# Optimization experiments

Hardware: AMD Instinct MI355X
Metric: run time of the kernel (lower is better)

## Reference

```python
import jax, jax.numpy as jnp
import numpy as np

INV_SQRT2 = 0.7071067811865476  # Haar/db1 filter coefficient
LEVEL = 3


def _split(x, axis):
    """One Haar analysis step along `axis` (even length assumed)."""
    ax = axis % x.ndim
    sl0 = [slice(None)] * x.ndim; sl0[ax] = slice(0, None, 2)
    sl1 = [slice(None)] * x.ndim; sl1[ax] = slice(1, None, 2)
    x0, x1 = x[tuple(sl0)], x[tuple(sl1)]
    return (x0 + x1) * INV_SQRT2, (x0 - x1) * INV_SQRT2


def _merge(lo, hi, axis):
    """One Haar synthesis step along `axis` (interleave even/odd)."""
    ax = axis % lo.ndim
    e = (lo + hi) * INV_SQRT2
    o = (lo - hi) * INV_SQRT2
    s = jnp.stack([e, o], axis=ax + 1)
    shape = list(lo.shape)
    shape[ax] *= 2
    return s.reshape(shape)


def _dwt2(x):
    lo, hi = _split(x, -1)
    a, h = _split(lo, -2)
    v, d = _split(hi, -2)
    return a, h, v, d


def _idwt2(a, h, v, d):
    lo = _merge(a, h, -2)
    hi = _merge(v, d, -2)
    return _merge(lo, hi, -1)


def setup_inputs() -> dict:
    key = jax.random.key(0)
    ks = jax.random.split(key, 8)
    B, H, W = 16, 1024, 1024
    x = jax.random.normal(ks[0], (B, H, W, 1), dtype=jnp.float32)
    na = (H // 8) * (W // 8)   # approx size at level 3
    n2 = (H // 4) * (W // 4)
    n1 = (H // 2) * (W // 2)
    scale = 0.02
    Wa = jax.random.normal(ks[1], (na, 1), dtype=jnp.float32) * scale
    ba = jnp.zeros((1,), jnp.float32)
    Wd1 = jax.random.normal(ks[2], (3 * na, 3), dtype=jnp.float32) * scale  # coarsest details
    bd1 = jnp.zeros((3,), jnp.float32)
    Wd2 = jax.random.normal(ks[3], (3 * n2, 3), dtype=jnp.float32) * scale
    bd2 = jnp.zeros((3,), jnp.float32)
    Wd3 = jax.random.normal(ks[4], (3 * n1, 3), dtype=jnp.float32) * scale  # finest details
    bd3 = jnp.zeros((3,), jnp.float32)
    return {"x": x, "Wa": Wa, "ba": ba, "Wd1": Wd1, "bd1": bd1,
            "Wd2": Wd2, "bd2": bd2, "Wd3": Wd3, "bd3": bd3}


def reference(x, Wa, ba, Wd1, bd1, Wd2, bd2, Wd3, bd3):
    img = x[..., 0]                      # [B, H, W]
    B = img.shape[0]
    details = []                         # finest -> coarsest
    cur = img
    for _ in range(LEVEL):
        cur, h, v, d = _dwt2(cur)
        details.append((h, v, d))
    # approximation attention: sigmoid(Dense(1)) scalar gate per sample
    aw = jax.nn.sigmoid(cur.reshape(B, -1) @ Wa + ba)   # [B, 1]
    rec = cur * aw[:, :, None]                           # [B, H/8, W/8]
    # detail attention per level (coarsest first, matching pywt coeff order)
    det_params = [(Wd1, bd1), (Wd2, bd2), (Wd3, bd3)]
    for (h, v, d), (Wd, bd) in zip(reversed(details), det_params):
        flat = jnp.stack([h, v, d], axis=1).reshape(B, -1)      # [B, 3*hl*wl]
        w = jax.nn.softmax(flat @ Wd + bd, axis=-1)             # [B, 3]
        rec = _idwt2(rec,
                     h * w[:, 0, None, None],
                     v * w[:, 1, None, None],
                     d * w[:, 2, None, None])
    return rec                                                   # [B, H, W]
```

## Files before the change

kernel.cpp:

```cpp
#include <hip/hip_runtime.h>
#include <math.h>

#define HH 1024
#define WW 1024
#define N1 262144
#define N2 65536
#define N3 16384
#define NCHUNK 4
#define ROWS_PER_IMG 512

#define C_INV_SQRT2 0.70710678118654752440f

static __device__ __forceinline__ void haar_fwd(float P, float Q, float R, float S,
                                                float& a, float& h, float& v, float& d) {
    const float C = C_INV_SQRT2;
    float lo0 = (P + Q) * C, lo1 = (R + S) * C;
    float hi0 = (P - Q) * C, hi1 = (R - S) * C;
    a = (lo0 + lo1) * C; h = (lo0 - lo1) * C;
    v = (hi0 + hi1) * C; d = (hi0 - hi1) * C;
}

static __device__ __forceinline__ void haar_inv(float a, float h, float v, float d,
                                                float& P, float& Q, float& R, float& S) {
    const float C = C_INV_SQRT2;
    float elo = (a + h) * C, olo = (a - h) * C;
    float ehi = (v + d) * C, ohi = (v - d) * C;
    P = (elo + ehi) * C; Q = (elo - ehi) * C;
    R = (olo + ohi) * C; S = (olo - ohi) * C;
}

__global__ __launch_bounds__(256) void wa_fwd_dots(
    const float* __restrict__ x,
    const float* __restrict__ Wa,
    const float* __restrict__ Wd1,
    const float* __restrict__ Wd2,
    const float* __restrict__ Wd3,
    float* __restrict__ partial,
    int ipc)
{
    const int strip = blockIdx.x;
    const int chunk = blockIdx.y;
    const int t = threadIdx.x;
    const int lane = t & 63, wave = t >> 6;

    float w1[3][4][6];
    #pragma unroll
    for (int qr = 0; qr < 4; ++qr) {
        const size_t jj = (size_t)(strip * 4 + qr) * 512 + 2 * t;
        #pragma unroll
        for (int s = 0; s < 3; ++s) {
            const float2* src = (const float2*)(Wd3 + (jj + (size_t)s * N1) * 3);
            float2 f0 = src[0], f1 = src[1], f2 = src[2];
            w1[s][qr][0] = f0.x; w1[s][qr][1] = f0.y; w1[s][qr][2] = f1.x;
            w1[s][qr][3] = f1.y; w1[s][qr][4] = f2.x; w1[s][qr][5] = f2.y;
        }
    }
    float w2[3][2][3];
    #pragma unroll
    for (int QR = 0; QR < 2; ++QR) {
        const size_t jj = (size_t)(strip * 2 + QR) * 256 + t;
        #pragma unroll
        for (int s = 0; s < 3; ++s) {
            const float* src = Wd2 + (jj + (size_t)s * N2) * 3;
            w2[s][QR][0] = src[0]; w2[s][QR][1] = src[1]; w2[s][QR][2] = src[2];
        }
    }
    float w3[3][3] = {};
    float wa = 0.f;
    if (!(t & 1)) {
        const size_t jj = (size_t)strip * 128 + (t >> 1);
        wa = Wa[jj];
        #pragma unroll
        for (int s = 0; s < 3; ++s) {
            const float* src = Wd1 + (jj + (size_t)s * N3) * 3;
            w3[s][0] = src[0]; w3[s][1] = src[1]; w3[s][2] = src[2];
        }
    }

    #pragma unroll 2
    for (int bi = 0; bi < ipc; ++bi) {
        const int b = chunk * ipc + bi;
        const float* xr = x + (size_t)b * HH * WW + (size_t)strip * 8 * WW + 4 * t;

        float acc[10];
        #pragma unroll
        for (int c = 0; c < 10; ++c) acc[c] = 0.f;

        float a1[4][2];
        #pragma unroll
        for (int qr = 0; qr < 4; ++qr) {
            float4 u0 = *(const float4*)(xr + (size_t)(2 * qr)     * WW);
            float4 u1 = *(const float4*)(xr + (size_t)(2 * qr + 1) * WW);
            float h_[2], v_[2], d_[2];
            haar_fwd(u0.x, u0.y, u1.x, u1.y, a1[qr][0], h_[0], v_[0], d_[0]);
            haar_fwd(u0.z, u0.w, u1.z, u1.w, a1[qr][1], h_[1], v_[1], d_[1]);
            #pragma unroll
            for (int qc = 0; qc < 2; ++qc)
                #pragma unroll
                for (int c = 0; c < 3; ++c)
                    acc[7 + c] += h_[qc] * w1[0][qr][qc * 3 + c]
                                + v_[qc] * w1[1][qr][qc * 3 + c]
                                + d_[qc] * w1[2][qr][qc * 3 + c];
        }

        float a2[2];
        #pragma unroll
        for (int QR = 0; QR < 2; ++QR) {
            float h2, v2, d2;
            haar_fwd(a1[2 * QR][0], a1[2 * QR][1], a1[2 * QR + 1][0], a1[2 * QR + 1][1],
                     a2[QR], h2, v2, d2);
            #pragma unroll
            for (int c = 0; c < 3; ++c)
                acc[4 + c] += h2 * w2[0][QR][c] + v2 * w2[1][QR][c] + d2 * w2[2][QR][c];
        }

        {
            float oa0 = __shfl_xor(a2[0], 1);
            float oa1 = __shfl_xor(a2[1], 1);
            if (!(t & 1)) {
                float a3, h3, v3, d3;
                haar_fwd(a2[0], oa0, a2[1], oa1, a3, h3, v3, d3);
                acc[0] += a3 * wa;
                #pragma unroll
                for (int c = 0; c < 3; ++c)
                    acc[1 + c] += h3 * w3[0][c] + v3 * w3[1][c] + d3 * w3[2][c];
            }
        }

        #pragma unroll
        for (int c = 0; c < 10; ++c) {
            float s = acc[c];
            #pragma unroll
            for (int off = 1; off < 64; off <<= 1) s += __shfl_xor(s, off);
            acc[c] = s;
        }
        if (lane == 0) {
            float* row = partial + ((size_t)b * ROWS_PER_IMG + (size_t)strip * 4 + wave) * 10;
            #pragma unroll
            for (int c = 0; c < 10; ++c) row[c] = acc[c];
        }
    }
}

__global__ __launch_bounds__(64) void wa_gates(
    const float* __restrict__ partial,
    const float* __restrict__ ba,
    const float* __restrict__ bd1,
    const float* __restrict__ bd2,
    const float* __restrict__ bd3,
    float* __restrict__ gates)
{
    const int b = blockIdx.x;
    const int l = threadIdx.x;
    float v[10];
    #pragma unroll
    for (int c = 0; c < 10; ++c) v[c] = 0.f;
    for (int r = l; r < ROWS_PER_IMG; r += 64) {
        const float* row = partial + ((size_t)b * ROWS_PER_IMG + r) * 10;
        #pragma unroll
        for (int c = 0; c < 10; ++c) v[c] += row[c];
    }
    #pragma unroll
    for (int c = 0; c < 10; ++c) {
        #pragma unroll
        for (int off = 1; off < 64; off <<= 1) v[c] += __shfl_xor(v[c], off);
    }
    if (l == 0) {
        float* G = gates + b * 10;
        G[0] = 1.f / (1.f + expf(-(v[0] + ba[0])));
        const float* bds[3] = { bd1, bd2, bd3 };
        #pragma unroll
        for (int lv = 0; lv < 3; ++lv) {
            float l0 = v[1 + 3 * lv + 0] + bds[lv][0];
            float l1 = v[1 + 3 * lv + 1] + bds[lv][1];
            float l2 = v[1 + 3 * lv + 2] + bds[lv][2];
            float m = fmaxf(l0, fmaxf(l1, l2));
            float e0 = expf(l0 - m), e1 = expf(l1 - m), e2 = expf(l2 - m);
            float inv = 1.f / (e0 + e1 + e2);
            G[1 + 3 * lv + 0] = e0 * inv;
            G[1 + 3 * lv + 1] = e1 * inv;
            G[1 + 3 * lv + 2] = e2 * inv;
        }
    }
}

__global__ __launch_bounds__(256) void wa_recon(
    const float* __restrict__ x,
    const float* __restrict__ gates,
    float* __restrict__ out)
{
    const int strip = blockIdx.x;
    const int b = blockIdx.y;
    const int t = threadIdx.x;

    __shared__ float g[10];
    if (t < 10) g[t] = gates[b * 10 + t];
    __syncthreads();

    const float* xr = x + (size_t)b * HH * WW + (size_t)strip * 8 * WW + 4 * t;

    float a1[4][2], h1[4][2], v1[4][2], d1[4][2];
    #pragma unroll
    for (int qr = 0; qr < 4; ++qr) {
        float4 u0 = *(const float4*)(xr + (size_t)(2 * qr)     * WW);
        float4 u1 = *(const float4*)(xr + (size_t)(2 * qr + 1) * WW);
        haar_fwd(u0.x, u0.y, u1.x, u1.y, a1[qr][0], h1[qr][0], v1[qr][0], d1[qr][0]);
        haar_fwd(u0.z, u0.w, u1.z, u1.w, a1[qr][1], h1[qr][1], v1[qr][1], d1[qr][1]);
    }
    float a2[2], h2[2], v2[2], d2[2];
    #pragma unroll
    for (int QR = 0; QR < 2; ++QR)
        haar_fwd(a1[2 * QR][0], a1[2 * QR][1], a1[2 * QR + 1][0], a1[2 * QR + 1][1],
                 a2[QR], h2[QR], v2[QR], d2[QR]);

    float oa0 = __shfl_xor(a2[0], 1);
    float oa1 = __shfl_xor(a2[1], 1);
    const bool rightside = t & 1;
    float a3, h3, v3, d3;
    if (!rightside) haar_fwd(a2[0], oa0, a2[1], oa1, a3, h3, v3, d3);
    else            haar_fwd(oa0, a2[0], oa1, a2[1], a3, h3, v3, d3);

    a3 *= g[0];
    float P, Q, R, S;
    haar_inv(a3, h3 * g[1], v3 * g[2], d3 * g[3], P, Q, R, S);
    float r2[2];
    r2[0] = rightside ? Q : P;
    r2[1] = rightside ? S : R;

    float ra1[4][2];
    #pragma unroll
    for (int QR = 0; QR < 2; ++QR) {
        haar_inv(r2[QR], h2[QR] * g[4], v2[QR] * g[5], d2[QR] * g[6], P, Q, R, S);
        ra1[2 * QR][0] = P; ra1[2 * QR][1] = Q;
        ra1[2 * QR + 1][0] = R; ra1[2 * QR + 1][1] = S;
    }

    float* orow = out + (size_t)b * HH * WW + (size_t)strip * 8 * WW + 4 * t;
    #pragma unroll
    for (int qr = 0; qr < 4; ++qr) {
        float4 o0, o1;
        haar_inv(ra1[qr][0], h1[qr][0] * g[7], v1[qr][0] * g[8], d1[qr][0] * g[9],
                 o0.x, o0.y, o1.x, o1.y);
        haar_inv(ra1[qr][1], h1[qr][1] * g[7], v1[qr][1] * g[8], d1[qr][1] * g[9],
                 o0.z, o0.w, o1.z, o1.w);
        *(float4*)(orow + (size_t)(2 * qr)     * WW) = o0;
        *(float4*)(orow + (size_t)(2 * qr + 1) * WW) = o1;
    }
}

extern "C" void kernel_launch(void* const* d_in, const int* in_sizes, int n_in,
                              void* d_out, int out_size, void* d_ws, size_t ws_size,
                              hipStream_t stream) {
    const float* x   = (const float*)d_in[0];
    const float* Wa  = (const float*)d_in[1];
    const float* ba  = (const float*)d_in[2];
    const float* Wd1 = (const float*)d_in[3];
    const float* bd1 = (const float*)d_in[4];
    const float* Wd2 = (const float*)d_in[5];
    const float* bd2 = (const float*)d_in[6];
    const float* Wd3 = (const float*)d_in[7];
    const float* bd3 = (const float*)d_in[8];
    float* out = (float*)d_out;

    const int B = in_sizes[0] / (HH * WW);

    float* partial = (float*)d_ws;
    float* gates   = partial + (size_t)B * ROWS_PER_IMG * 10;

    int nchunk = NCHUNK, ipc = B / NCHUNK;
    if (B % NCHUNK) { nchunk = B; ipc = 1; }

    dim3 fgrid(128, nchunk);
    wa_fwd_dots<<<fgrid, 256, 0, stream>>>(x, Wa, Wd1, Wd2, Wd3, partial, ipc);
    wa_gates<<<B, 64, 0, stream>>>(partial, ba, bd1, bd2, bd3, gates);
    dim3 rgrid(128, B);
    wa_recon<<<rgrid, 256, 0, stream>>>(x, gates, out);
}
```

Measured before the change: 155.2 us.

## Fuse forward dots, gate computation and reconstruction into one cooperative kernel

Replaces the three-kernel sequence (forward dot products, gate softmax, reconstruction) with a single cooperative kernel that uses a grid-wide sync between the reduction phase and the reconstruction phase. Weights stay in registers, each block computes the gates for its own images redundantly after the sync, and then reconstructs directly. This removes two kernel launches and the separate gate kernel, at the cost of a grid barrier and a 512-block cooperative launch that must be fully co-resident. The old three-kernel path remains as a fallback if the cooperative launch fails.

```diff
diff --git a/kernel.cpp b/kernel.cpp
--- a/kernel.cpp
+++ b/kernel.cpp
@@ -1,4 +1,5 @@
 #include <hip/hip_runtime.h>
+#include <hip/hip_cooperative_groups.h>
 #include <math.h>
 
 #define HH 1024
@@ -8,8 +9,11 @@
 #define N3 16384
 #define NCHUNK 4
 #define ROWS_PER_IMG 512
+#define MAX_IPC 8
 
 #define C_INV_SQRT2 0.70710678118654752440f
+
+namespace cg = cooperative_groups;
 
 static __device__ __forceinline__ void haar_fwd(float P, float Q, float R, float S,
                                                 float& a, float& h, float& v, float& d) {
@@ -27,6 +31,232 @@
     float ehi = (v + d) * C, ohi = (v - d) * C;
     P = (elo + ehi) * C; Q = (elo - ehi) * C;
     R = (olo + ohi) * C; S = (olo - ohi) * C;
+}
+
+__global__ __launch_bounds__(256, 2) void wa_fused(
+    const float* __restrict__ x,
+    const float* __restrict__ Wa,
+    const float* __restrict__ ba,
+    const float* __restrict__ Wd1,
+    const float* __restrict__ bd1,
+    const float* __restrict__ Wd2,
+    const float* __restrict__ bd2,
+    const float* __restrict__ Wd3,
+    const float* __restrict__ bd3,
+    float* __restrict__ partial,
+    float* __restrict__ out,
+    int ipc)
+{
+    const int strip = blockIdx.x;
+    const int chunk = blockIdx.y;
+    const int t = threadIdx.x;
+    const int lane = t & 63, wave = t >> 6;
+
+    __shared__ float smP[MAX_IPC][16][10];
+    __shared__ float smG[2][10];
+    __shared__ float gl[10];
+
+    float w1[3][4][6];
+    #pragma unroll
+    for (int qr = 0; qr < 4; ++qr) {
+        const size_t jj = (size_t)(strip * 4 + qr) * 512 + 2 * t;
+        #pragma unroll
+        for (int s = 0; s < 3; ++s) {
+            const float2* src = (const float2*)(Wd3 + (jj + (size_t)s * N1) * 3);
+            float2 f0 = src[0], f1 = src[1], f2 = src[2];
+            w1[s][qr][0] = f0.x; w1[s][qr][1] = f0.y; w1[s][qr][2] = f1.x;
+            w1[s][qr][3] = f1.y; w1[s][qr][4] = f2.x; w1[s][qr][5] = f2.y;
+        }
+    }
+    float w2[3][2][3];
+    #pragma unroll
+    for (int QR = 0; QR < 2; ++QR) {
+        const size_t jj = (size_t)(strip * 2 + QR) * 256 + t;
+        #pragma unroll
+        for (int s = 0; s < 3; ++s) {
+            const float* src = Wd2 + (jj + (size_t)s * N2) * 3;
+            w2[s][QR][0] = src[0]; w2[s][QR][1] = src[1]; w2[s][QR][2] = src[2];
+        }
+    }
+    float w3[3][3] = {};
+    float wa = 0.f;
+    if (!(t & 1)) {
+        const size_t jj = (size_t)strip * 128 + (t >> 1);
+        wa = Wa[jj];
+        #pragma unroll
+        for (int s = 0; s < 3; ++s) {
+            const float* src = Wd1 + (jj + (size_t)s * N3) * 3;
+            w3[s][0] = src[0]; w3[s][1] = src[1]; w3[s][2] = src[2];
+        }
+    }
+
+    #pragma unroll 2
+    for (int bi = 0; bi < ipc; ++bi) {
+        const int b = chunk * ipc + bi;
+        const float* xr = x + (size_t)b * HH * WW + (size_t)strip * 8 * WW + 4 * t;
+
+        float acc[10];
+        #pragma unroll
+        for (int c = 0; c < 10; ++c) acc[c] = 0.f;
+
+        float a1[4][2];
+        #pragma unroll
+        for (int qr = 0; qr < 4; ++qr) {
+            float4 u0 = *(const float4*)(xr + (size_t)(2 * qr)     * WW);
+            float4 u1 = *(const float4*)(xr + (size_t)(2 * qr + 1) * WW);
+            float h_[2], v_[2], d_[2];
+            haar_fwd(u0.x, u0.y, u1.x, u1.y, a1[qr][0], h_[0], v_[0], d_[0]);
+            haar_fwd(u0.z, u0.w, u1.z, u1.w, a1[qr][1], h_[1], v_[1], d_[1]);
+            #pragma unroll
+            for (int qc = 0; qc < 2; ++qc)
+                #pragma unroll
+                for (int c = 0; c < 3; ++c)
+                    acc[7 + c] += h_[qc] * w1[0][qr][qc * 3 + c]
+                                + v_[qc] * w1[1][qr][qc * 3 + c]
+                                + d_[qc] * w1[2][qr][qc * 3 + c];
+        }
+
+        float a2[2];
+        #pragma unroll
+        for (int QR = 0; QR < 2; ++QR) {
+            float h2, v2, d2;
+            haar_fwd(a1[2 * QR][0], a1[2 * QR][1], a1[2 * QR + 1][0], a1[2 * QR + 1][1],
+                     a2[QR], h2, v2, d2);
+            #pragma unroll
+            for (int c = 0; c < 3; ++c)
+                acc[4 + c] += h2 * w2[0][QR][c] + v2 * w2[1][QR][c] + d2 * w2[2][QR][c];
+        }
+
+        {
+            float oa0 = __shfl_xor(a2[0], 1);
+            float oa1 = __shfl_xor(a2[1], 1);
+            if (!(t & 1)) {
+                float a3, h3, v3, d3;
+                haar_fwd(a2[0], oa0, a2[1], oa1, a3, h3, v3, d3);
+                acc[0] += a3 * wa;
+                #pragma unroll
+                for (int c = 0; c < 3; ++c)
+                    acc[1 + c] += h3 * w3[0][c] + v3 * w3[1][c] + d3 * w3[2][c];
+            }
+        }
+
+        #pragma unroll
+        for (int c = 0; c < 10; ++c) {
+            float s = acc[c];
+            s += __shfl_xor(s, 1);
+            s += __shfl_xor(s, 2);
+            s += __shfl_xor(s, 4);
+            s += __shfl_xor(s, 8);
+            acc[c] = s;
+        }
+        const int sel = lane & 15;
+        float vsel = acc[0];
+        #pragma unroll
+        for (int c = 1; c < 10; ++c) vsel = (sel == c) ? acc[c] : vsel;
+        if (sel < 10) smP[bi][(wave << 2) | (lane >> 4)][sel] = vsel;
+    }
+    __syncthreads();
+    if (t < ipc * 10) {
+        const int bi = t / 10, c = t - bi * 10;
+        float s = 0.f;
+        #pragma unroll
+        for (int j = 0; j < 16; ++j) s += smP[bi][j][c];
+        partial[((size_t)(chunk * ipc + bi) * 128 + strip) * 10 + c] = s;
+    }
+
+    __threadfence();
+    cg::this_grid().sync();
+
+    for (int bi = 0; bi < ipc; ++bi) {
+        const int b = chunk * ipc + bi;
+
+        if (t < 128) {
+            const float* row = partial + ((size_t)b * 128 + t) * 10;
+            float v[10];
+            #pragma unroll
+            for (int c = 0; c < 10; ++c) v[c] = row[c];
+            #pragma unroll
+            for (int c = 0; c < 10; ++c) {
+                #pragma unroll
+                for (int off = 1; off < 64; off <<= 1) v[c] += __shfl_xor(v[c], off);
+            }
+            if (lane == 0) {
+                #pragma unroll
+                for (int c = 0; c < 10; ++c) smG[wave][c] = v[c];
+            }
+        }
+        __syncthreads();
+        if (t == 0) {
+            const float* bds[3] = { bd1, bd2, bd3 };
+            float s0 = smG[0][0] + smG[1][0];
+            gl[0] = 1.f / (1.f + expf(-(s0 + ba[0])));
+            #pragma unroll
+            for (int lv = 0; lv < 3; ++lv) {
+                float l0 = smG[0][1 + 3 * lv + 0] + smG[1][1 + 3 * lv + 0] + bds[lv][0];
+                float l1 = smG[0][1 + 3 * lv + 1] + smG[1][1 + 3 * lv + 1] + bds[lv][1];
+                float l2 = smG[0][1 + 3 * lv + 2] + smG[1][1 + 3 * lv + 2] + bds[lv][2];
+                float m = fmaxf(l0, fmaxf(l1, l2));
+                float e0 = expf(l0 - m), e1 = expf(l1 - m), e2 = expf(l2 - m);
+                float inv = 1.f / (e0 + e1 + e2);
+                gl[1 + 3 * lv + 0] = e0 * inv;
+                gl[1 + 3 * lv + 1] = e1 * inv;
+                gl[1 + 3 * lv + 2] = e2 * inv;
+            }
+        }
+        __syncthreads();
+        float gv[10];
+        #pragma unroll
+        for (int c = 0; c < 10; ++c) gv[c] = gl[c];
+
+        const float* xr = x + (size_t)b * HH * WW + (size_t)strip * 8 * WW + 4 * t;
+        float a1r[4][2], h1[4][2], v1[4][2], d1[4][2];
+        #pragma unroll
+        for (int qr = 0; qr < 4; ++qr) {
+            float4 u0 = *(const float4*)(xr + (size_t)(2 * qr)     * WW);
+            float4 u1 = *(const float4*)(xr + (size_t)(2 * qr + 1) * WW);
+            haar_fwd(u0.x, u0.y, u1.x, u1.y, a1r[qr][0], h1[qr][0], v1[qr][0], d1[qr][0]);
+            haar_fwd(u0.z, u0.w, u1.z, u1.w, a1r[qr][1], h1[qr][1], v1[qr][1], d1[qr][1]);
+        }
+        float a2r[2], h2[2], v2[2], d2[2];
+        #pragma unroll
+        for (int QR = 0; QR < 2; ++QR)
+            haar_fwd(a1r[2 * QR][0], a1r[2 * QR][1], a1r[2 * QR + 1][0], a1r[2 * QR + 1][1],
+                     a2r[QR], h2[QR], v2[QR], d2[QR]);
+
+        float oa0 = __shfl_xor(a2r[0], 1);
+        float oa1 = __shfl_xor(a2r[1], 1);
+        const bool rightside = t & 1;
+        float a3, h3, v3, d3;
+        if (!rightside) haar_fwd(a2r[0], oa0, a2r[1], oa1, a3, h3, v3, d3);
+        else            haar_fwd(oa0, a2r[0], oa1, a2r[1], a3, h3, v3, d3);
+
+        a3 *= gv[0];
+        float P, Q, R, S;
+        haar_inv(a3, h3 * gv[1], v3 * gv[2], d3 * gv[3], P, Q, R, S);
+        float r2[2];
+        r2[0] = rightside ? Q : P;
+        r2[1] = rightside ? S : R;
+
+        float ra1[4][2];
+        #pragma unroll
+        for (int QR = 0; QR < 2; ++QR) {
+            haar_inv(r2[QR], h2[QR] * gv[4], v2[QR] * gv[5], d2[QR] * gv[6], P, Q, R, S);
+            ra1[2 * QR][0] = P; ra1[2 * QR][1] = Q;
+            ra1[2 * QR + 1][0] = R; ra1[2 * QR + 1][1] = S;
+        }
+
+        float* orow = out + (size_t)b * HH * WW + (size_t)strip * 8 * WW + 4 * t;
+        #pragma unroll
+        for (int qr = 0; qr < 4; ++qr) {
+            float4 o0, o1;
+            haar_inv(ra1[qr][0], h1[qr][0] * gv[7], v1[qr][0] * gv[8], d1[qr][0] * gv[9],
+                     o0.x, o0.y, o1.x, o1.y);
+            haar_inv(ra1[qr][1], h1[qr][1] * gv[7], v1[qr][1] * gv[8], d1[qr][1] * gv[9],
+                     o0.z, o0.w, o1.z, o1.w);
+            *(float4*)(orow + (size_t)(2 * qr)     * WW) = o0;
+            *(float4*)(orow + (size_t)(2 * qr + 1) * WW) = o1;
+        }
+    }
 }
 
 __global__ __launch_bounds__(256) void wa_fwd_dots(
@@ -267,6 +497,20 @@
     float* partial = (float*)d_ws;
     float* gates   = partial + (size_t)B * ROWS_PER_IMG * 10;
 
+    if ((B % NCHUNK) == 0 && (B / NCHUNK) <= MAX_IPC) {
+        int ipcv = B / NCHUNK;
+        const float* xa  = x;   const float* Waa = Wa;  const float* baa = ba;
+        const float* w1a = Wd1; const float* b1a = bd1;
+        const float* w2a = Wd2; const float* b2a = bd2;
+        const float* w3a = Wd3; const float* b3a = bd3;
+        float* pa = partial; float* oa = out;
+        void* args[] = { &xa, &Waa, &baa, &w1a, &b1a, &w2a, &b2a, &w3a, &b3a,
+                         &pa, &oa, &ipcv };
+        hipError_t e = hipLaunchCooperativeKernel(wa_fused, dim3(128, NCHUNK),
+                                                  dim3(256, 1, 1), args, 0u, stream);
+        if (e == hipSuccess) return;
+    }
+
     int nchunk = NCHUNK, ipc = B / NCHUNK;
     if (B % NCHUNK) { nchunk = B; ipc = 1; }
 
```

Result: slower. 270.4 us (+74.2%).

## Reload weights per image instead of caching in registers, raise occupancy and chunk count

Applied to the files above, without the earlier changes.

Drops the per-thread register cache of the Wd1/Wd2/Wd3/Wa weights and reloads them from global memory inside the per-image loop. Also raises the chunk count from 4 to 16 and adds a minimum-occupancy launch bound. The aim is lower register pressure, more resident waves and more blocks to hide the latency of the x stream. The cost is repeated weight loads for every image, which the grid split only partly offsets with fewer images per block, and more partial-sum traffic if the chunk layout changes.

```diff
diff --git a/kernel.cpp b/kernel.cpp
--- a/kernel.cpp
+++ b/kernel.cpp
@@ -6,7 +6,7 @@
 #define N1 262144
 #define N2 65536
 #define N3 16384
-#define NCHUNK 4
+#define NCHUNK 16
 #define ROWS_PER_IMG 512
 
 #define C_INV_SQRT2 0.70710678118654752440f
@@ -29,7 +29,7 @@
     R = (olo + ohi) * C; S = (olo - ohi) * C;
 }
 
-__global__ __launch_bounds__(256) void wa_fwd_dots(
+__global__ __launch_bounds__(256, 6) void wa_fwd_dots(
     const float* __restrict__ x,
     const float* __restrict__ Wa,
     const float* __restrict__ Wd1,
@@ -43,41 +43,6 @@
     const int t = threadIdx.x;
     const int lane = t & 63, wave = t >> 6;
 
-    float w1[3][4][6];
-    #pragma unroll
-    for (int qr = 0; qr < 4; ++qr) {
-        const size_t jj = (size_t)(strip * 4 + qr) * 512 + 2 * t;
-        #pragma unroll
-        for (int s = 0; s < 3; ++s) {
-            const float2* src = (const float2*)(Wd3 + (jj + (size_t)s * N1) * 3);
-            float2 f0 = src[0], f1 = src[1], f2 = src[2];
-            w1[s][qr][0] = f0.x; w1[s][qr][1] = f0.y; w1[s][qr][2] = f1.x;
-            w1[s][qr][3] = f1.y; w1[s][qr][4] = f2.x; w1[s][qr][5] = f2.y;
-        }
-    }
-    float w2[3][2][3];
-    #pragma unroll
-    for (int QR = 0; QR < 2; ++QR) {
-        const size_t jj = (size_t)(strip * 2 + QR) * 256 + t;
-        #pragma unroll
-        for (int s = 0; s < 3; ++s) {
-            const float* src = Wd2 + (jj + (size_t)s * N2) * 3;
-            w2[s][QR][0] = src[0]; w2[s][QR][1] = src[1]; w2[s][QR][2] = src[2];
-        }
-    }
-    float w3[3][3] = {};
-    float wa = 0.f;
-    if (!(t & 1)) {
-        const size_t jj = (size_t)strip * 128 + (t >> 1);
-        wa = Wa[jj];
-        #pragma unroll
-        for (int s = 0; s < 3; ++s) {
-            const float* src = Wd1 + (jj + (size_t)s * N3) * 3;
-            w3[s][0] = src[0]; w3[s][1] = src[1]; w3[s][2] = src[2];
-        }
-    }
-
-    #pragma unroll 2
     for (int bi = 0; bi < ipc; ++bi) {
         const int b = chunk * ipc + bi;
         const float* xr = x + (size_t)b * HH * WW + (size_t)strip * 8 * WW + 4 * t;
@@ -94,13 +59,29 @@
             float h_[2], v_[2], d_[2];
             haar_fwd(u0.x, u0.y, u1.x, u1.y, a1[qr][0], h_[0], v_[0], d_[0]);
             haar_fwd(u0.z, u0.w, u1.z, u1.w, a1[qr][1], h_[1], v_[1], d_[1]);
-            #pragma unroll
-            for (int qc = 0; qc < 2; ++qc)
-                #pragma unroll
-                for (int c = 0; c < 3; ++c)
-                    acc[7 + c] += h_[qc] * w1[0][qr][qc * 3 + c]
-                                + v_[qc] * w1[1][qr][qc * 3 + c]
-                                + d_[qc] * w1[2][qr][qc * 3 + c];
+
+            const size_t jj = (size_t)(strip * 4 + qr) * 512 + 2 * t;
+            {
+                const float2* src = (const float2*)(Wd3 + jj * 3);
+                float2 f0 = src[0], f1 = src[1], f2 = src[2];
+                acc[7] += h_[0] * f0.x + h_[1] * f1.y;
+                acc[8] += h_[0] * f0.y + h_[1] * f2.x;
+                acc[9] += h_[0] * f1.x + h_[1] * f2.y;
+            }
+            {
+                const float2* src = (const float2*)(Wd3 + (jj + (size_t)N1) * 3);
+                float2 f0 = src[0], f1 = src[1], f2 = src[2];
+                acc[7] += v_[0] * f0.x + v_[1] * f1.y;
+                acc[8] += v_[0] * f0.y + v_[1] * f2.x;
+                acc[9] += v_[0] * f1.x + v_[1] * f2.y;
+            }
+            {
+                const float2* src = (const float2*)(Wd3 + (jj + (size_t)(2 * N1)) * 3);
+                float2 f0 = src[0], f1 = src[1], f2 = src[2];
+                acc[7] += d_[0] * f0.x + d_[1] * f1.y;
+                acc[8] += d_[0] * f0.y + d_[1] * f2.x;
+                acc[9] += d_[0] * f1.x + d_[1] * f2.y;
+            }
         }
 
         float a2[2];
@@ -109,9 +90,13 @@
             float h2, v2, d2;
             haar_fwd(a1[2 * QR][0], a1[2 * QR][1], a1[2 * QR + 1][0], a1[2 * QR + 1][1],
                      a2[QR], h2, v2, d2);
+            const size_t jj = (size_t)(strip * 2 + QR) * 256 + t;
+            const float* s0 = Wd2 + jj * 3;
+            const float* s1 = Wd2 + (jj + (size_t)N2) * 3;
+            const float* s2 = Wd2 + (jj + (size_t)(2 * N2)) * 3;
             #pragma unroll
             for (int c = 0; c < 3; ++c)
-                acc[4 + c] += h2 * w2[0][QR][c] + v2 * w2[1][QR][c] + d2 * w2[2][QR][c];
+                acc[4 + c] += h2 * s0[c] + v2 * s1[c] + d2 * s2[c];
         }
 
         {
@@ -120,10 +105,14 @@
             if (!(t & 1)) {
                 float a3, h3, v3, d3;
                 haar_fwd(a2[0], oa0, a2[1], oa1, a3, h3, v3, d3);
-                acc[0] += a3 * wa;
+                const size_t jj = (size_t)strip * 128 + (t >> 1);
+                acc[0] += a3 * Wa[jj];
+                const float* s0 = Wd1 + jj * 3;
+                const float* s1 = Wd1 + (jj + (size_t)N3) * 3;
+                const float* s2 = Wd1 + (jj + (size_t)(2 * N3)) * 3;
                 #pragma unroll
                 for (int c = 0; c < 3; ++c)
-                    acc[1 + c] += h3 * w3[0][c] + v3 * w3[1][c] + d3 * w3[2][c];
+                    acc[1 + c] += h3 * s0[c] + v3 * s1[c] + d3 * s2[c];
             }
         }
 
```

Measured after the change: 274.8 us. +77.0%, slower.
